# Performance work log

Hardware: AMD Instinct MI355X
Metric: run time of the kernel (lower is better)

## Reference

```python
import jax, jax.numpy as jnp
import numpy as np

N, H, F, E, K = 4096, 512, 2048, 8, 2  # tokens, hidden, ffn(=4H), experts, top_k


def setup_inputs() -> dict:
    key = jax.random.key(0)
    ks = jax.random.split(key, 7)
    def w(k, shape, fan_in):
        return jax.random.normal(k, shape, dtype=jnp.float32) * (fan_in ** -0.5)
    return {
        "x": jax.random.normal(ks[0], (N, H), dtype=jnp.float32),
        "W_in": w(ks[1], (H, H), H),          # input_proj.weight  [out,in]
        "W_router": w(ks[2], (E, H), H),      # router.gate.weight [E,H]
        "W_gate": w(ks[3], (E, F, H), H),     # per-expert gate_proj.weight
        "W_up": w(ks[4], (E, F, H), H),       # per-expert up_proj.weight
        "W_down": w(ks[5], (E, H, F), F),     # per-expert down_proj.weight
        "W_out": w(ks[6], (H, H), H),         # output_proj.weight
    }


def reference(x, W_in, W_router, W_gate, W_up, W_down, W_out):
    h = x @ W_in.T                                  # [N,H] input_proj
    logits = h @ W_router.T                         # [N,E]
    # route_mode='balanced' and world_size==1 -> expert_bias is None
    probs = jax.nn.softmax(logits, axis=-1)
    top_w, top_i = jax.lax.top_k(probs, K)          # [N,K]
    top_w = jax.nn.softmax(top_w, axis=-1)          # renormalize over top-k

    # per-token combine weight for each expert: [N,E]
    onehot = jax.nn.one_hot(top_i, E, dtype=h.dtype)      # [N,K,E]
    combine_w = jnp.einsum('nk,nke->ne', top_w, onehot)

    def expert(wg, wu, wd):
        # SwiGLU FFN: down( silu(gate(h)) * up(h) )
        return (jax.nn.silu(h @ wg.T) * (h @ wu.T)) @ wd.T  # [N,H]

    expert_out = jax.vmap(expert)(W_gate, W_up, W_down)     # [E,N,H]
    combined = jnp.einsum('ne,enh->nh', combine_w, expert_out)
    return combined @ W_out.T                                # output_proj
```

## Files before the change

kernel.cpp:

```cpp
#include <hip/hip_runtime.h>

typedef unsigned short u16;
typedef unsigned int u32;
typedef short bf16x8 __attribute__((ext_vector_type(8)));
typedef float f32x4 __attribute__((ext_vector_type(4)));

#define AS1 __attribute__((address_space(1)))
#define AS3 __attribute__((address_space(3)))

#define NTOK 4096
#define HDIM 512
#define FDIM 2048
#define NEXP 8
#define TOPK 2
#define NASSIGN (NTOK * TOPK)
#define NPAD (NASSIGN + NEXP * 128)
#define RBMAX 128

__device__ __forceinline__ void g2l16(const void* g, void* l) {
  __builtin_amdgcn_global_load_lds((const AS1 u32*)g, (AS3 u32*)l, 16, 0, 0);
}

__device__ __forceinline__ u16 f2bf(float f) {
  u32 u = __float_as_uint(f);
  u = (u + 0x7FFFu + ((u >> 16) & 1u)) >> 16;
  return (u16)u;
}

__global__ void cvt_kernel(const float* __restrict__ src, u16* __restrict__ dst, int n4) {
  int i = blockIdx.x * blockDim.x + threadIdx.x;
  if (i >= n4) return;
  float4 v = reinterpret_cast<const float4*>(src)[i];
  ushort4 o;
  o.x = f2bf(v.x); o.y = f2bf(v.y); o.z = f2bf(v.z); o.w = f2bf(v.w);
  reinterpret_cast<ushort4*>(dst)[i] = o;
}

__global__ void wreff_kernel(const float* __restrict__ Wr, const float* __restrict__ Win,
                             double* __restrict__ wre) {
  int t = blockIdx.x * blockDim.x + threadIdx.x;
  int e = t >> 9, k = t & 511;
  const float* wr = Wr + e * HDIM;
  double a = 0.0;
  for (int j = 0; j < HDIM; ++j) a += (double)wr[j] * (double)Win[j * HDIM + k];
  wre[t] = a;
}

__global__ __launch_bounds__(256) void router_kernel(
    const float* __restrict__ x, const double* __restrict__ wre,
    int* __restrict__ idx, float* __restrict__ wts) {
  __shared__ double lw[NEXP * HDIM];
  for (int i = threadIdx.x; i < NEXP * HDIM; i += 256) lw[i] = wre[i];
  __syncthreads();
  int n = blockIdx.x * 256 + threadIdx.x;
  const float* xr = x + (size_t)n * HDIM;
  double acc[NEXP] = {};
  for (int k = 0; k < HDIM; ++k) {
    double xv = (double)xr[k];
#pragma unroll
    for (int e = 0; e < NEXP; ++e) acc[e] += xv * lw[e * HDIM + k];
  }
  double mx = acc[0];
#pragma unroll
  for (int e = 1; e < NEXP; ++e) mx = acc[e] > mx ? acc[e] : mx;
  double p[NEXP], se = 0.0;
#pragma unroll
  for (int e = 0; e < NEXP; ++e) { p[e] = exp(acc[e] - mx); se += p[e]; }
  double inv = 1.0 / se;
#pragma unroll
  for (int e = 0; e < NEXP; ++e) p[e] *= inv;
  int i0 = 0; double b0 = p[0];
#pragma unroll
  for (int e = 1; e < NEXP; ++e) if (p[e] > b0) { b0 = p[e]; i0 = e; }
  int i1 = -1; double b1 = -1.0;
#pragma unroll
  for (int e = 0; e < NEXP; ++e) if (e != i0 && p[e] > b1) { b1 = p[e]; i1 = e; }
  double e0 = exp(b0), e1 = exp(b1);
  idx[2 * n] = i0; idx[2 * n + 1] = i1;
  wts[2 * n] = (float)(e0 / (e0 + e1));
  wts[2 * n + 1] = (float)(e1 / (e0 + e1));
}

__global__ void assign_kernel(const int* __restrict__ idx, int* __restrict__ tok,
                              int* __restrict__ pos, int* __restrict__ rbe,
                              int* __restrict__ rbp, int* __restrict__ nrb) {
  __shared__ int cnt[NEXP], cur[NEXP];
  const int tid = threadIdx.x;
  if (tid < NEXP) cnt[tid] = 0;
  __syncthreads();
  for (int a = tid; a < NASSIGN; a += 256) atomicAdd(&cnt[idx[a]], 1);
  __syncthreads();
  if (tid == 0) {
    int o = 0, n = 0;
    for (int e = 0; e < NEXP; ++e) {
      cur[e] = o;
      int nb = (cnt[e] + 127) >> 7;
      for (int i = 0; i < nb; ++i) { rbe[n] = e; rbp[n] = o + i * 128; ++n; }
      o += nb * 128;
    }
    nrb[0] = n;
  }
  __syncthreads();
  for (int p = tid; p < NPAD; p += 256) tok[p] = 0;
  __syncthreads();
  for (int a = tid; a < NASSIGN; a += 256) {
    int e = idx[a];
    int q = atomicAdd(&cur[e], 1);
    tok[q] = a >> 1;
    pos[a] = q;
  }
}

template <int STORE_BF16>
__global__ __launch_bounds__(256, 2) void gemm_bt_kernel(
    const u16* __restrict__ A, const u16* __restrict__ B, void* __restrict__ C,
    int M, int N, int K) {
  __shared__ u16 lA[128 * 64];
  __shared__ u16 lB[128 * 64];
  const int tid = threadIdx.x;
  const int w = tid >> 6, l = tid & 63;
  const int m0 = blockIdx.y * 128, n0 = blockIdx.x * 128;
  const int wm = (w >> 1) * 64, wn = (w & 1) * 64;
  const int lr = l >> 3, lc = (l & 7) * 8;
  f32x4 acc[4][4] = {};
  const u16* Ab = A + (size_t)(m0 + w * 32 + lr) * K + lc;
  const u16* Bb = B + (size_t)(n0 + w * 32 + lr) * K + lc;
  for (int kt = 0; kt < K; kt += 64) {
#pragma unroll
    for (int j = 0; j < 4; ++j) {
      g2l16(Ab + (size_t)j * 8 * K + kt, &lA[w * 2048 + j * 512]);
      g2l16(Bb + (size_t)j * 8 * K + kt, &lB[w * 2048 + j * 512]);
    }
    __syncthreads();
#pragma unroll
    for (int kk = 0; kk < 2; ++kk) {
      bf16x8 af[4], bf[4];
      const int ko = kk * 32 + (l >> 4) * 8;
#pragma unroll
      for (int i = 0; i < 4; ++i) af[i] = *(const bf16x8*)&lA[(wm + i * 16 + (l & 15)) * 64 + ko];
#pragma unroll
      for (int j = 0; j < 4; ++j) bf[j] = *(const bf16x8*)&lB[(wn + j * 16 + (l & 15)) * 64 + ko];
#pragma unroll
      for (int i = 0; i < 4; ++i)
#pragma unroll
        for (int j = 0; j < 4; ++j)
          acc[i][j] = __builtin_amdgcn_mfma_f32_16x16x32_bf16(af[i], bf[j], acc[i][j], 0, 0, 0);
    }
    __syncthreads();
  }
  const int cr = (l >> 4) * 4, cc = l & 15;
#pragma unroll
  for (int i = 0; i < 4; ++i)
#pragma unroll
    for (int j = 0; j < 4; ++j)
#pragma unroll
      for (int r = 0; r < 4; ++r) {
        int row = m0 + wm + i * 16 + cr + r;
        int col = n0 + wn + j * 16 + cc;
        if (STORE_BF16)
          ((u16*)C)[(size_t)row * N + col] = f2bf(acc[i][j][r]);
        else
          ((float*)C)[(size_t)row * N + col] = acc[i][j][r];
      }
}

__global__ __launch_bounds__(256, 2) void gateup_kernel(
    const u16* __restrict__ hb, const u16* __restrict__ Wg, const u16* __restrict__ Wu,
    u16* __restrict__ act, const int* __restrict__ tok, const int* __restrict__ rbe,
    const int* __restrict__ rbp, const int* __restrict__ nrb) {
  const int rb = blockIdx.y;
  if (rb >= nrb[0]) return;
  __shared__ u16 lA[128 * 64];
  __shared__ u16 lG[128 * 64];
  __shared__ u16 lU[128 * 64];
  const int e = rbe[rb], p0 = rbp[rb], n0 = blockIdx.x * 128;
  const int tid = threadIdx.x;
  const int w = tid >> 6, l = tid & 63;
  const int wm = (w >> 1) * 64, wn = (w & 1) * 64;
  const int lr = l >> 3, lc = (l & 7) * 8;
  const u16* Bg = Wg + (size_t)e * (FDIM * HDIM) + (size_t)(n0 + w * 32 + lr) * HDIM + lc;
  const u16* Bu = Wu + (size_t)e * (FDIM * HDIM) + (size_t)(n0 + w * 32 + lr) * HDIM + lc;
  int trow[4];
#pragma unroll
  for (int j = 0; j < 4; ++j) trow[j] = tok[p0 + w * 32 + j * 8 + lr];
  f32x4 ag[4][4] = {}, au[4][4] = {};
  for (int kt = 0; kt < HDIM; kt += 64) {
#pragma unroll
    for (int j = 0; j < 4; ++j) {
      g2l16(hb + (size_t)trow[j] * HDIM + kt + lc, &lA[w * 2048 + j * 512]);
      g2l16(Bg + (size_t)j * 8 * HDIM + kt, &lG[w * 2048 + j * 512]);
      g2l16(Bu + (size_t)j * 8 * HDIM + kt, &lU[w * 2048 + j * 512]);
    }
    __syncthreads();
#pragma unroll
    for (int kk = 0; kk < 2; ++kk) {
      bf16x8 af[4], gf[4], uf[4];
      const int ko = kk * 32 + (l >> 4) * 8;
#pragma unroll
      for (int i = 0; i < 4; ++i) af[i] = *(const bf16x8*)&lA[(wm + i * 16 + (l & 15)) * 64 + ko];
#pragma unroll
      for (int j = 0; j < 4; ++j) {
        gf[j] = *(const bf16x8*)&lG[(wn + j * 16 + (l & 15)) * 64 + ko];
        uf[j] = *(const bf16x8*)&lU[(wn + j * 16 + (l & 15)) * 64 + ko];
      }
#pragma unroll
      for (int i = 0; i < 4; ++i)
#pragma unroll
        for (int j = 0; j < 4; ++j) {
          ag[i][j] = __builtin_amdgcn_mfma_f32_16x16x32_bf16(af[i], gf[j], ag[i][j], 0, 0, 0);
          au[i][j] = __builtin_amdgcn_mfma_f32_16x16x32_bf16(af[i], uf[j], au[i][j], 0, 0, 0);
        }
    }
    __syncthreads();
  }
  const int cr = (l >> 4) * 4, cc = l & 15;
#pragma unroll
  for (int i = 0; i < 4; ++i)
#pragma unroll
    for (int j = 0; j < 4; ++j)
#pragma unroll
      for (int r = 0; r < 4; ++r) {
        int prow = p0 + wm + i * 16 + cr + r;
        int col = n0 + wn + j * 16 + cc;
        float g = ag[i][j][r], u = au[i][j][r];
        float s = g / (1.0f + __expf(-g));
        act[(size_t)prow * FDIM + col] = f2bf(s * u);
      }
}

__global__ __launch_bounds__(256, 2) void down_kernel(
    const u16* __restrict__ act, const u16* __restrict__ Wd, float* __restrict__ dout,
    const int* __restrict__ rbe, const int* __restrict__ rbp, const int* __restrict__ nrb) {
  const int rb = blockIdx.y;
  if (rb >= nrb[0]) return;
  __shared__ u16 lA[128 * 64];
  __shared__ u16 lB[128 * 64];
  const int e = rbe[rb], p0 = rbp[rb], n0 = blockIdx.x * 128;
  const int tid = threadIdx.x;
  const int w = tid >> 6, l = tid & 63;
  const int wm = (w >> 1) * 64, wn = (w & 1) * 64;
  const int lr = l >> 3, lc = (l & 7) * 8;
  f32x4 acc[4][4] = {};
  const u16* Ab = act + (size_t)(p0 + w * 32 + lr) * FDIM + lc;
  const u16* Bb = Wd + (size_t)e * (HDIM * FDIM) + (size_t)(n0 + w * 32 + lr) * FDIM + lc;
  for (int kt = 0; kt < FDIM; kt += 64) {
#pragma unroll
    for (int j = 0; j < 4; ++j) {
      g2l16(Ab + (size_t)j * 8 * FDIM + kt, &lA[w * 2048 + j * 512]);
      g2l16(Bb + (size_t)j * 8 * FDIM + kt, &lB[w * 2048 + j * 512]);
    }
    __syncthreads();
#pragma unroll
    for (int kk = 0; kk < 2; ++kk) {
      bf16x8 af[4], bf[4];
      const int ko = kk * 32 + (l >> 4) * 8;
#pragma unroll
      for (int i = 0; i < 4; ++i) af[i] = *(const bf16x8*)&lA[(wm + i * 16 + (l & 15)) * 64 + ko];
#pragma unroll
      for (int j = 0; j < 4; ++j) bf[j] = *(const bf16x8*)&lB[(wn + j * 16 + (l & 15)) * 64 + ko];
#pragma unroll
      for (int i = 0; i < 4; ++i)
#pragma unroll
        for (int j = 0; j < 4; ++j)
          acc[i][j] = __builtin_amdgcn_mfma_f32_16x16x32_bf16(af[i], bf[j], acc[i][j], 0, 0, 0);
    }
    __syncthreads();
  }
  const int cr = (l >> 4) * 4, cc = l & 15;
#pragma unroll
  for (int i = 0; i < 4; ++i)
#pragma unroll
    for (int j = 0; j < 4; ++j)
#pragma unroll
      for (int r = 0; r < 4; ++r) {
        int prow = p0 + wm + i * 16 + cr + r;
        int col = n0 + wn + j * 16 + cc;
        dout[(size_t)prow * HDIM + col] = acc[i][j][r];
      }
}

__global__ void combine_kernel(const float* __restrict__ dout, const int* __restrict__ pos,
                               const float* __restrict__ wts, u16* __restrict__ cb) {
  const int n = blockIdx.x, t = threadIdx.x;
  const int p0 = pos[2 * n], p1 = pos[2 * n + 1];
  const float w0 = wts[2 * n], w1 = wts[2 * n + 1];
  const float4 a = reinterpret_cast<const float4*>(dout + (size_t)p0 * HDIM)[t];
  const float4 b = reinterpret_cast<const float4*>(dout + (size_t)p1 * HDIM)[t];
  ushort4 o;
  o.x = f2bf(w0 * a.x + w1 * b.x);
  o.y = f2bf(w0 * a.y + w1 * b.y);
  o.z = f2bf(w0 * a.z + w1 * b.z);
  o.w = f2bf(w0 * a.w + w1 * b.w);
  reinterpret_cast<ushort4*>(cb + (size_t)n * HDIM)[t] = o;
}

extern "C" void kernel_launch(void* const* d_in, const int* in_sizes, int n_in,
                              void* d_out, int out_size, void* d_ws, size_t ws_size,
                              hipStream_t stream) {
  const float* x   = (const float*)d_in[0];
  const float* Wi  = (const float*)d_in[1];
  const float* Wr  = (const float*)d_in[2];
  const float* Wg  = (const float*)d_in[3];
  const float* Wu  = (const float*)d_in[4];
  const float* Wd  = (const float*)d_in[5];
  const float* Wo  = (const float*)d_in[6];
  float* out = (float*)d_out;

  char* ws = (char*)d_ws;
  size_t off = 0;
  auto alloc = [&](size_t bytes) -> void* {
    off = (off + 255) & ~(size_t)255;
    void* p = ws + off;
    off += bytes;
    return p;
  };
  u16* xb  = (u16*)alloc((size_t)NTOK * HDIM * 2);
  u16* hb  = (u16*)alloc((size_t)NTOK * HDIM * 2);
  u16* cb  = (u16*)alloc((size_t)NTOK * HDIM * 2);
  u16* Wib = (u16*)alloc((size_t)HDIM * HDIM * 2);
  u16* Wob = (u16*)alloc((size_t)HDIM * HDIM * 2);
  u16* Wgb = (u16*)alloc((size_t)NEXP * FDIM * HDIM * 2);
  u16* Wub = (u16*)alloc((size_t)NEXP * FDIM * HDIM * 2);
  u16* Wdb = (u16*)alloc((size_t)NEXP * HDIM * FDIM * 2);
  u16* actb = (u16*)alloc((size_t)NPAD * FDIM * 2);
  float* dwn = (float*)alloc((size_t)NPAD * HDIM * 4);
  double* wre = (double*)alloc((size_t)NEXP * HDIM * 8);
  int* idx = (int*)alloc((size_t)NASSIGN * 4);
  float* wts = (float*)alloc((size_t)NASSIGN * 4);
  int* tok = (int*)alloc((size_t)NPAD * 4);
  int* pos = (int*)alloc((size_t)NASSIGN * 4);
  int* rbe = (int*)alloc((size_t)RBMAX * 4);
  int* rbp = (int*)alloc((size_t)RBMAX * 4);
  int* nrb = (int*)alloc(256);

  auto cvt = [&](const float* s, u16* d, size_t n) {
    int n4 = (int)(n / 4);
    cvt_kernel<<<(n4 + 255) / 256, 256, 0, stream>>>(s, d, n4);
  };
  cvt(x, xb, (size_t)NTOK * HDIM);
  cvt(Wi, Wib, (size_t)HDIM * HDIM);
  cvt(Wg, Wgb, (size_t)NEXP * FDIM * HDIM);
  cvt(Wu, Wub, (size_t)NEXP * FDIM * HDIM);
  cvt(Wd, Wdb, (size_t)NEXP * HDIM * FDIM);
  cvt(Wo, Wob, (size_t)HDIM * HDIM);

  wreff_kernel<<<(NEXP * HDIM) / 256, 256, 0, stream>>>(Wr, Wi, wre);
  gemm_bt_kernel<1><<<dim3(HDIM / 128, NTOK / 128), 256, 0, stream>>>(xb, Wib, hb, NTOK, HDIM, HDIM);
  router_kernel<<<NTOK / 256, 256, 0, stream>>>(x, wre, idx, wts);
  assign_kernel<<<1, 256, 0, stream>>>(idx, tok, pos, rbe, rbp, nrb);
  gateup_kernel<<<dim3(FDIM / 128, 72), 256, 0, stream>>>(hb, Wgb, Wub, actb, tok, rbe, rbp, nrb);
  down_kernel<<<dim3(HDIM / 128, 72), 256, 0, stream>>>(actb, Wdb, dwn, rbe, rbp, nrb);
  combine_kernel<<<NTOK, 128, 0, stream>>>(dwn, pos, wts, cb);
  gemm_bt_kernel<0><<<dim3(HDIM / 128, NTOK / 128), 256, 0, stream>>>(cb, Wob, out, NTOK, HDIM, HDIM);
}
```

Baseline: 251.5 us.

## Fuse prep kernels, double-buffer GEMMs with swizzled LDS, store down output in bf16

Merges the separate conversion, router-weight, input-projection and router launches into two multi-role prep kernels, so independent work shares one launch. Rewrites all GEMMs to use 512-thread blocks, double-buffered LDS with an XOR swizzle, and a prefetch of the next k-tile during MFMA compute. The down projection now covers a wider 256-column tile and stores bf16 instead of fp32, which halves the intermediate traffic that combine reads. In exchange the down output carries extra rounding, and each block needs more LDS.

```diff
diff --git a/kernel.cpp b/kernel.cpp
--- a/kernel.cpp
+++ b/kernel.cpp
@@ -12,73 +12,166 @@
 #define HDIM 512
 #define FDIM 2048
 #define NEXP 8
-#define TOPK 2
-#define NASSIGN (NTOK * TOPK)
+#define NASSIGN (NTOK * 2)
 #define NPAD (NASSIGN + NEXP * 128)
 #define RBMAX 128
 
 __device__ __forceinline__ void g2l16(const void* g, void* l) {
   __builtin_amdgcn_global_load_lds((const AS1 u32*)g, (AS3 u32*)l, 16, 0, 0);
 }
-
 __device__ __forceinline__ u16 f2bf(float f) {
   u32 u = __float_as_uint(f);
   u = (u + 0x7FFFu + ((u >> 16) & 1u)) >> 16;
   return (u16)u;
 }
-
-__global__ void cvt_kernel(const float* __restrict__ src, u16* __restrict__ dst, int n4) {
-  int i = blockIdx.x * blockDim.x + threadIdx.x;
-  if (i >= n4) return;
-  float4 v = reinterpret_cast<const float4*>(src)[i];
-  ushort4 o;
-  o.x = f2bf(v.x); o.y = f2bf(v.y); o.z = f2bf(v.z); o.w = f2bf(v.w);
-  reinterpret_cast<ushort4*>(dst)[i] = o;
-}
-
-__global__ void wreff_kernel(const float* __restrict__ Wr, const float* __restrict__ Win,
-                             double* __restrict__ wre) {
-  int t = blockIdx.x * blockDim.x + threadIdx.x;
-  int e = t >> 9, k = t & 511;
-  const float* wr = Wr + e * HDIM;
-  double a = 0.0;
-  for (int j = 0; j < HDIM; ++j) a += (double)wr[j] * (double)Win[j * HDIM + k];
-  wre[t] = a;
-}
-
-__global__ __launch_bounds__(256) void router_kernel(
+__device__ __forceinline__ float bf2f(u16 h) { return __uint_as_float(((u32)h) << 16); }
+
+#define VMBAR() do { asm volatile("s_waitcnt vmcnt(0)" ::: "memory"); __builtin_amdgcn_s_barrier(); } while (0)
+
+__global__ __launch_bounds__(512, 4) void prep1_kernel(
+    const float* __restrict__ x, const float* __restrict__ Wi, const float* __restrict__ Wo,
+    const float* __restrict__ Wr, u16* __restrict__ xb, u16* __restrict__ Wib,
+    u16* __restrict__ Wob, double* __restrict__ wre) {
+  const int b = blockIdx.x, tid = threadIdx.x;
+  if (b < 640) {
+    const float* s; u16* d; int base;
+    if (b < 512) { s = x; d = xb; base = b * 1024; }
+    else if (b < 576) { s = Wi; d = Wib; base = (b - 512) * 1024; }
+    else { s = Wo; d = Wob; base = (b - 576) * 1024; }
+#pragma unroll
+    for (int i = 0; i < 2; ++i) {
+      const int ix = base + tid + i * 512;
+      const float4 v = ((const float4*)s)[ix];
+      ushort4 o; o.x = f2bf(v.x); o.y = f2bf(v.y); o.z = f2bf(v.z); o.w = f2bf(v.w);
+      ((ushort4*)d)[ix] = o;
+    }
+  } else {
+    const int t = (b - 640) * 512 + tid;
+    const int e = t >> 9, k = t & 511;
+    const float* wr = Wr + e * HDIM;
+    double a = 0.0;
+    for (int j = 0; j < HDIM; ++j) a += (double)wr[j] * (double)Wi[j * HDIM + k];
+    wre[t] = a;
+  }
+}
+
+template <int SB, int NT>
+__device__ __forceinline__ void gemm128_body(
+    const u16* __restrict__ A, const u16* __restrict__ B, void* __restrict__ C,
+    int m0, int n0, int N, int K, u16* sm, int tid) {
+  u16 *lA0 = sm, *lA1 = sm + 8192, *lB0 = sm + 16384, *lB1 = sm + 24576;
+  const int w = tid >> 6, l = tid & 63;
+  const int wm = (w >> 2) * 64, wn = (w & 3) * 32;
+  const int lm = l & 15, lk = (l >> 4) * 8, xr = (l & 7) << 3;
+  const int sr = l >> 3, sc = ((l & 7) ^ sr) * 8;
+  const u16* As = A + (size_t)(m0 + w * 8 + sr) * K + sc;
+  const u16* Bs = B + (size_t)(n0 + w * 8 + sr) * K + sc;
+  f32x4 acc[4][2] = {};
+  auto STG = [&](u16* dA, u16* dB, int kt) {
+    g2l16(As + kt, dA + w * 512);
+    g2l16(As + (size_t)64 * K + kt, dA + 4096 + w * 512);
+    g2l16(Bs + kt, dB + w * 512);
+    g2l16(Bs + (size_t)64 * K + kt, dB + 4096 + w * 512);
+  };
+  auto CMP = [&](const u16* a_, const u16* b_) {
+#pragma unroll
+    for (int kk = 0; kk < 2; ++kk) {
+      const int ko = (kk * 32 + lk) ^ xr;
+      bf16x8 af[4], bf[2];
+#pragma unroll
+      for (int i = 0; i < 4; ++i) af[i] = *(const bf16x8*)(a_ + (wm + i * 16 + lm) * 64 + ko);
+#pragma unroll
+      for (int j = 0; j < 2; ++j) bf[j] = *(const bf16x8*)(b_ + (wn + j * 16 + lm) * 64 + ko);
+#pragma unroll
+      for (int i = 0; i < 4; ++i)
+#pragma unroll
+        for (int j = 0; j < 2; ++j)
+          acc[i][j] = __builtin_amdgcn_mfma_f32_16x16x32_bf16(af[i], bf[j], acc[i][j], 0, 0, 0);
+    }
+  };
+  STG(lA0, lB0, 0);
+  VMBAR();
+  for (int t = 0; t < NT; t += 2) {
+    if (t + 1 < NT) STG(lA1, lB1, (t + 1) * 64);
+    CMP(lA0, lB0);
+    VMBAR();
+    if (t + 2 < NT) STG(lA0, lB0, (t + 2) * 64);
+    CMP(lA1, lB1);
+    VMBAR();
+  }
+  const int cr = (l >> 4) * 4, cc = lm;
+#pragma unroll
+  for (int i = 0; i < 4; ++i)
+#pragma unroll
+    for (int j = 0; j < 2; ++j)
+#pragma unroll
+      for (int r = 0; r < 4; ++r) {
+        const size_t o = (size_t)(m0 + wm + i * 16 + cr + r) * N + n0 + wn + j * 16 + cc;
+        if (SB) ((u16*)C)[o] = f2bf(acc[i][j][r]);
+        else ((float*)C)[o] = acc[i][j][r];
+      }
+}
+
+__global__ __launch_bounds__(512, 4) void prep2_kernel(
     const float* __restrict__ x, const double* __restrict__ wre,
+    const u16* __restrict__ xb, const u16* __restrict__ Wib,
+    const float* __restrict__ Wg, const float* __restrict__ Wu, const float* __restrict__ Wd,
+    u16* __restrict__ hb, u16* __restrict__ Wgb, u16* __restrict__ Wub, u16* __restrict__ Wdb,
     int* __restrict__ idx, float* __restrict__ wts) {
-  __shared__ double lw[NEXP * HDIM];
-  for (int i = threadIdx.x; i < NEXP * HDIM; i += 256) lw[i] = wre[i];
-  __syncthreads();
-  int n = blockIdx.x * 256 + threadIdx.x;
-  const float* xr = x + (size_t)n * HDIM;
-  double acc[NEXP] = {};
-  for (int k = 0; k < HDIM; ++k) {
-    double xv = (double)xr[k];
-#pragma unroll
-    for (int e = 0; e < NEXP; ++e) acc[e] += xv * lw[e * HDIM + k];
-  }
-  double mx = acc[0];
-#pragma unroll
-  for (int e = 1; e < NEXP; ++e) mx = acc[e] > mx ? acc[e] : mx;
-  double p[NEXP], se = 0.0;
-#pragma unroll
-  for (int e = 0; e < NEXP; ++e) { p[e] = exp(acc[e] - mx); se += p[e]; }
-  double inv = 1.0 / se;
-#pragma unroll
-  for (int e = 0; e < NEXP; ++e) p[e] *= inv;
-  int i0 = 0; double b0 = p[0];
-#pragma unroll
-  for (int e = 1; e < NEXP; ++e) if (p[e] > b0) { b0 = p[e]; i0 = e; }
-  int i1 = -1; double b1 = -1.0;
-#pragma unroll
-  for (int e = 0; e < NEXP; ++e) if (e != i0 && p[e] > b1) { b1 = p[e]; i1 = e; }
-  double e0 = exp(b0), e1 = exp(b1);
-  idx[2 * n] = i0; idx[2 * n + 1] = i1;
-  wts[2 * n] = (float)(e0 / (e0 + e1));
-  wts[2 * n + 1] = (float)(e1 / (e0 + e1));
+  __shared__ __align__(16) u16 pp[32768];
+  const int b = blockIdx.x, tid = threadIdx.x;
+  if (b < 8) {
+    double* lw = (double*)pp;
+    for (int i = tid; i < NEXP * HDIM; i += 512) lw[i] = wre[i];
+    __syncthreads();
+    const int n = b * 512 + tid;
+    const float* xr = x + (size_t)n * HDIM;
+    double acc[NEXP] = {};
+    for (int k4 = 0; k4 < HDIM / 4; ++k4) {
+      const float4 xv = ((const float4*)xr)[k4];
+      const float xc[4] = {xv.x, xv.y, xv.z, xv.w};
+#pragma unroll
+      for (int c = 0; c < 4; ++c) {
+        const double xd = (double)xc[c];
+#pragma unroll
+        for (int e = 0; e < NEXP; ++e) acc[e] += xd * lw[e * HDIM + k4 * 4 + c];
+      }
+    }
+    double mx = acc[0];
+#pragma unroll
+    for (int e = 1; e < NEXP; ++e) mx = acc[e] > mx ? acc[e] : mx;
+    double p[NEXP], se = 0.0;
+#pragma unroll
+    for (int e = 0; e < NEXP; ++e) { p[e] = exp(acc[e] - mx); se += p[e]; }
+    const double inv = 1.0 / se;
+#pragma unroll
+    for (int e = 0; e < NEXP; ++e) p[e] *= inv;
+    int i0 = 0; double b0 = p[0];
+#pragma unroll
+    for (int e = 1; e < NEXP; ++e) if (p[e] > b0) { b0 = p[e]; i0 = e; }
+    int i1 = -1; double b1 = -1.0;
+#pragma unroll
+    for (int e = 0; e < NEXP; ++e) if (e != i0 && p[e] > b1) { b1 = p[e]; i1 = e; }
+    const double e0 = exp(b0), e1 = exp(b1);
+    idx[2 * n] = i0; idx[2 * n + 1] = i1;
+    wts[2 * n] = (float)(e0 / (e0 + e1));
+    wts[2 * n + 1] = (float)(e1 / (e0 + e1));
+  } else if (b < 136) {
+    const int g = b - 8;
+    gemm128_body<1, 8>(xb, Wib, hb, (g >> 2) * 128, (g & 3) * 128, HDIM, HDIM, pp, tid);
+  } else {
+    const int cb = b - 136, which = cb >> 9, lb = cb & 511;
+    const float* s = which == 0 ? Wg : which == 1 ? Wu : Wd;
+    u16* d = which == 0 ? Wgb : which == 1 ? Wub : Wdb;
+    const int base = lb * 4096 + tid;
+#pragma unroll
+    for (int i = 0; i < 8; ++i) {
+      const int ix = base + i * 512;
+      const float4 v = ((const float4*)s)[ix];
+      ushort4 o; o.x = f2bf(v.x); o.y = f2bf(v.y); o.z = f2bf(v.z); o.w = f2bf(v.w);
+      ((ushort4*)d)[ix] = o;
+    }
+  }
 }
 
 __global__ void assign_kernel(const int* __restrict__ idx, int* __restrict__ tok,
@@ -94,7 +187,7 @@
     int o = 0, n = 0;
     for (int e = 0; e < NEXP; ++e) {
       cur[e] = o;
-      int nb = (cnt[e] + 127) >> 7;
+      const int nb = (cnt[e] + 127) >> 7;
       for (int i = 0; i < nb; ++i) { rbe[n] = e; rbp[n] = o + i * 128; ++n; }
       o += nb * 128;
     }
@@ -104,206 +197,176 @@
   for (int p = tid; p < NPAD; p += 256) tok[p] = 0;
   __syncthreads();
   for (int a = tid; a < NASSIGN; a += 256) {
-    int e = idx[a];
-    int q = atomicAdd(&cur[e], 1);
+    const int e = idx[a];
+    const int q = atomicAdd(&cur[e], 1);
     tok[q] = a >> 1;
     pos[a] = q;
   }
 }
 
-template <int STORE_BF16>
-__global__ __launch_bounds__(256, 2) void gemm_bt_kernel(
-    const u16* __restrict__ A, const u16* __restrict__ B, void* __restrict__ C,
-    int M, int N, int K) {
-  __shared__ u16 lA[128 * 64];
-  __shared__ u16 lB[128 * 64];
-  const int tid = threadIdx.x;
-  const int w = tid >> 6, l = tid & 63;
-  const int m0 = blockIdx.y * 128, n0 = blockIdx.x * 128;
-  const int wm = (w >> 1) * 64, wn = (w & 1) * 64;
-  const int lr = l >> 3, lc = (l & 7) * 8;
-  f32x4 acc[4][4] = {};
-  const u16* Ab = A + (size_t)(m0 + w * 32 + lr) * K + lc;
-  const u16* Bb = B + (size_t)(n0 + w * 32 + lr) * K + lc;
-  for (int kt = 0; kt < K; kt += 64) {
-#pragma unroll
-    for (int j = 0; j < 4; ++j) {
-      g2l16(Ab + (size_t)j * 8 * K + kt, &lA[w * 2048 + j * 512]);
-      g2l16(Bb + (size_t)j * 8 * K + kt, &lB[w * 2048 + j * 512]);
-    }
-    __syncthreads();
-#pragma unroll
-    for (int kk = 0; kk < 2; ++kk) {
-      bf16x8 af[4], bf[4];
-      const int ko = kk * 32 + (l >> 4) * 8;
-#pragma unroll
-      for (int i = 0; i < 4; ++i) af[i] = *(const bf16x8*)&lA[(wm + i * 16 + (l & 15)) * 64 + ko];
-#pragma unroll
-      for (int j = 0; j < 4; ++j) bf[j] = *(const bf16x8*)&lB[(wn + j * 16 + (l & 15)) * 64 + ko];
-#pragma unroll
-      for (int i = 0; i < 4; ++i)
-#pragma unroll
-        for (int j = 0; j < 4; ++j)
-          acc[i][j] = __builtin_amdgcn_mfma_f32_16x16x32_bf16(af[i], bf[j], acc[i][j], 0, 0, 0);
-    }
-    __syncthreads();
-  }
-  const int cr = (l >> 4) * 4, cc = l & 15;
-#pragma unroll
-  for (int i = 0; i < 4; ++i)
-#pragma unroll
-    for (int j = 0; j < 4; ++j)
-#pragma unroll
-      for (int r = 0; r < 4; ++r) {
-        int row = m0 + wm + i * 16 + cr + r;
-        int col = n0 + wn + j * 16 + cc;
-        if (STORE_BF16)
-          ((u16*)C)[(size_t)row * N + col] = f2bf(acc[i][j][r]);
-        else
-          ((float*)C)[(size_t)row * N + col] = acc[i][j][r];
-      }
-}
-
-__global__ __launch_bounds__(256, 2) void gateup_kernel(
+__global__ __launch_bounds__(512, 2) void gateup_kernel(
     const u16* __restrict__ hb, const u16* __restrict__ Wg, const u16* __restrict__ Wu,
     u16* __restrict__ act, const int* __restrict__ tok, const int* __restrict__ rbe,
     const int* __restrict__ rbp, const int* __restrict__ nrb) {
   const int rb = blockIdx.y;
   if (rb >= nrb[0]) return;
-  __shared__ u16 lA[128 * 64];
-  __shared__ u16 lG[128 * 64];
-  __shared__ u16 lU[128 * 64];
+  __shared__ __align__(16) u16 sm[49152];
+  u16 *lA0 = sm, *lA1 = sm + 8192, *lG0 = sm + 16384, *lG1 = sm + 24576,
+      *lU0 = sm + 32768, *lU1 = sm + 40960;
   const int e = rbe[rb], p0 = rbp[rb], n0 = blockIdx.x * 128;
-  const int tid = threadIdx.x;
-  const int w = tid >> 6, l = tid & 63;
-  const int wm = (w >> 1) * 64, wn = (w & 1) * 64;
-  const int lr = l >> 3, lc = (l & 7) * 8;
-  const u16* Bg = Wg + (size_t)e * (FDIM * HDIM) + (size_t)(n0 + w * 32 + lr) * HDIM + lc;
-  const u16* Bu = Wu + (size_t)e * (FDIM * HDIM) + (size_t)(n0 + w * 32 + lr) * HDIM + lc;
-  int trow[4];
-#pragma unroll
-  for (int j = 0; j < 4; ++j) trow[j] = tok[p0 + w * 32 + j * 8 + lr];
-  f32x4 ag[4][4] = {}, au[4][4] = {};
-  for (int kt = 0; kt < HDIM; kt += 64) {
-#pragma unroll
-    for (int j = 0; j < 4; ++j) {
-      g2l16(hb + (size_t)trow[j] * HDIM + kt + lc, &lA[w * 2048 + j * 512]);
-      g2l16(Bg + (size_t)j * 8 * HDIM + kt, &lG[w * 2048 + j * 512]);
-      g2l16(Bu + (size_t)j * 8 * HDIM + kt, &lU[w * 2048 + j * 512]);
-    }
-    __syncthreads();
+  const int tid = threadIdx.x, w = tid >> 6, l = tid & 63;
+  const int wm = (w >> 2) * 64, wn = (w & 3) * 32;
+  const int lm = l & 15, lk = (l >> 4) * 8, xr = (l & 7) << 3;
+  const int sr = l >> 3, sc = ((l & 7) ^ sr) * 8;
+  const u16* A0 = hb + (size_t)tok[p0 + w * 8 + sr] * HDIM + sc;
+  const u16* A1 = hb + (size_t)tok[p0 + 64 + w * 8 + sr] * HDIM + sc;
+  const u16* G0 = Wg + (size_t)e * FDIM * HDIM + (size_t)(n0 + w * 8 + sr) * HDIM + sc;
+  const u16* G1 = G0 + (size_t)64 * HDIM;
+  const u16* U0 = Wu + (size_t)e * FDIM * HDIM + (size_t)(n0 + w * 8 + sr) * HDIM + sc;
+  const u16* U1 = U0 + (size_t)64 * HDIM;
+  f32x4 ag[4][2] = {}, au[4][2] = {};
+  auto STG = [&](u16* dA, u16* dG, u16* dU, int kt) {
+    g2l16(A0 + kt, dA + w * 512);
+    g2l16(A1 + kt, dA + 4096 + w * 512);
+    g2l16(G0 + kt, dG + w * 512);
+    g2l16(G1 + kt, dG + 4096 + w * 512);
+    g2l16(U0 + kt, dU + w * 512);
+    g2l16(U1 + kt, dU + 4096 + w * 512);
+  };
+  auto CMP = [&](const u16* a_, const u16* g_, const u16* u_) {
 #pragma unroll
     for (int kk = 0; kk < 2; ++kk) {
-      bf16x8 af[4], gf[4], uf[4];
-      const int ko = kk * 32 + (l >> 4) * 8;
-#pragma unroll
-      for (int i = 0; i < 4; ++i) af[i] = *(const bf16x8*)&lA[(wm + i * 16 + (l & 15)) * 64 + ko];
-#pragma unroll
-      for (int j = 0; j < 4; ++j) {
-        gf[j] = *(const bf16x8*)&lG[(wn + j * 16 + (l & 15)) * 64 + ko];
-        uf[j] = *(const bf16x8*)&lU[(wn + j * 16 + (l & 15)) * 64 + ko];
+      const int ko = (kk * 32 + lk) ^ xr;
+      bf16x8 af[4], gf[2], uf[2];
+#pragma unroll
+      for (int i = 0; i < 4; ++i) af[i] = *(const bf16x8*)(a_ + (wm + i * 16 + lm) * 64 + ko);
+#pragma unroll
+      for (int j = 0; j < 2; ++j) {
+        gf[j] = *(const bf16x8*)(g_ + (wn + j * 16 + lm) * 64 + ko);
+        uf[j] = *(const bf16x8*)(u_ + (wn + j * 16 + lm) * 64 + ko);
       }
 #pragma unroll
       for (int i = 0; i < 4; ++i)
 #pragma unroll
-        for (int j = 0; j < 4; ++j) {
+        for (int j = 0; j < 2; ++j) {
           ag[i][j] = __builtin_amdgcn_mfma_f32_16x16x32_bf16(af[i], gf[j], ag[i][j], 0, 0, 0);
           au[i][j] = __builtin_amdgcn_mfma_f32_16x16x32_bf16(af[i], uf[j], au[i][j], 0, 0, 0);
         }
     }
-    __syncthreads();
-  }
-  const int cr = (l >> 4) * 4, cc = l & 15;
+  };
+  STG(lA0, lG0, lU0, 0);
+  VMBAR();
+#pragma unroll
+  for (int t = 0; t < 8; t += 2) {
+    if (t + 1 < 8) STG(lA1, lG1, lU1, (t + 1) * 64);
+    CMP(lA0, lG0, lU0);
+    VMBAR();
+    if (t + 2 < 8) STG(lA0, lG0, lU0, (t + 2) * 64);
+    CMP(lA1, lG1, lU1);
+    VMBAR();
+  }
+  const int cr = (l >> 4) * 4, cc = lm;
 #pragma unroll
   for (int i = 0; i < 4; ++i)
 #pragma unroll
-    for (int j = 0; j < 4; ++j)
+    for (int j = 0; j < 2; ++j)
 #pragma unroll
       for (int r = 0; r < 4; ++r) {
-        int prow = p0 + wm + i * 16 + cr + r;
-        int col = n0 + wn + j * 16 + cc;
-        float g = ag[i][j][r], u = au[i][j][r];
-        float s = g / (1.0f + __expf(-g));
-        act[(size_t)prow * FDIM + col] = f2bf(s * u);
+        const float g = ag[i][j][r], u = au[i][j][r];
+        const float s = g / (1.0f + __expf(-g));
+        act[(size_t)(p0 + wm + i * 16 + cr + r) * FDIM + n0 + wn + j * 16 + cc] = f2bf(s * u);
       }
 }
 
-__global__ __launch_bounds__(256, 2) void down_kernel(
-    const u16* __restrict__ act, const u16* __restrict__ Wd, float* __restrict__ dout,
+__global__ __launch_bounds__(512, 2) void down_kernel(
+    const u16* __restrict__ act, const u16* __restrict__ Wd, u16* __restrict__ dwn,
     const int* __restrict__ rbe, const int* __restrict__ rbp, const int* __restrict__ nrb) {
   const int rb = blockIdx.y;
   if (rb >= nrb[0]) return;
-  __shared__ u16 lA[128 * 64];
-  __shared__ u16 lB[128 * 64];
-  const int e = rbe[rb], p0 = rbp[rb], n0 = blockIdx.x * 128;
-  const int tid = threadIdx.x;
-  const int w = tid >> 6, l = tid & 63;
-  const int wm = (w >> 1) * 64, wn = (w & 1) * 64;
-  const int lr = l >> 3, lc = (l & 7) * 8;
+  __shared__ __align__(16) u16 sm[49152];
+  u16 *lA0 = sm, *lA1 = sm + 8192, *lB0 = sm + 16384, *lB1 = sm + 32768;
+  const int e = rbe[rb], p0 = rbp[rb], n0 = blockIdx.x * 256;
+  const int tid = threadIdx.x, w = tid >> 6, l = tid & 63;
+  const int wm = (w >> 2) * 64, wn = (w & 3) * 64;
+  const int lm = l & 15, lk = (l >> 4) * 8, xr = (l & 7) << 3;
+  const int sr = l >> 3, sc = ((l & 7) ^ sr) * 8;
+  const u16* As = act + (size_t)(p0 + w * 8 + sr) * FDIM + sc;
+  const u16* Bs = Wd + (size_t)e * HDIM * FDIM + (size_t)(n0 + w * 8 + sr) * FDIM + sc;
   f32x4 acc[4][4] = {};
-  const u16* Ab = act + (size_t)(p0 + w * 32 + lr) * FDIM + lc;
-  const u16* Bb = Wd + (size_t)e * (HDIM * FDIM) + (size_t)(n0 + w * 32 + lr) * FDIM + lc;
-  for (int kt = 0; kt < FDIM; kt += 64) {
-#pragma unroll
-    for (int j = 0; j < 4; ++j) {
-      g2l16(Ab + (size_t)j * 8 * FDIM + kt, &lA[w * 2048 + j * 512]);
-      g2l16(Bb + (size_t)j * 8 * FDIM + kt, &lB[w * 2048 + j * 512]);
-    }
-    __syncthreads();
+  auto STG = [&](u16* dA, u16* dB, int kt) {
+    g2l16(As + kt, dA + w * 512);
+    g2l16(As + (size_t)64 * FDIM + kt, dA + 4096 + w * 512);
+#pragma unroll
+    for (int c = 0; c < 4; ++c)
+      g2l16(Bs + (size_t)(64 * c) * FDIM + kt, dB + c * 4096 + w * 512);
+  };
+  auto CMP = [&](const u16* a_, const u16* b_) {
 #pragma unroll
     for (int kk = 0; kk < 2; ++kk) {
+      const int ko = (kk * 32 + lk) ^ xr;
       bf16x8 af[4], bf[4];
-      const int ko = kk * 32 + (l >> 4) * 8;
-#pragma unroll
-      for (int i = 0; i < 4; ++i) af[i] = *(const bf16x8*)&lA[(wm + i * 16 + (l & 15)) * 64 + ko];
-#pragma unroll
-      for (int j = 0; j < 4; ++j) bf[j] = *(const bf16x8*)&lB[(wn + j * 16 + (l & 15)) * 64 + ko];
+#pragma unroll
+      for (int i = 0; i < 4; ++i) af[i] = *(const bf16x8*)(a_ + (wm + i * 16 + lm) * 64 + ko);
+#pragma unroll
+      for (int j = 0; j < 4; ++j) bf[j] = *(const bf16x8*)(b_ + (wn + j * 16 + lm) * 64 + ko);
 #pragma unroll
       for (int i = 0; i < 4; ++i)
 #pragma unroll
         for (int j = 0; j < 4; ++j)
           acc[i][j] = __builtin_amdgcn_mfma_f32_16x16x32_bf16(af[i], bf[j], acc[i][j], 0, 0, 0);
     }
-    __syncthreads();
-  }
-  const int cr = (l >> 4) * 4, cc = l & 15;
+  };
+  STG(lA0, lB0, 0);
+  VMBAR();
+  for (int t = 0; t < 32; t += 2) {
+    if (t + 1 < 32) STG(lA1, lB1, (t + 1) * 64);
+    CMP(lA0, lB0);
+    VMBAR();
+    if (t + 2 < 32) STG(lA0, lB0, (t + 2) * 64);
+    CMP(lA1, lB1);
+    VMBAR();
+  }
+  const int cr = (l >> 4) * 4, cc = lm;
 #pragma unroll
   for (int i = 0; i < 4; ++i)
 #pragma unroll
     for (int j = 0; j < 4; ++j)
 #pragma unroll
-      for (int r = 0; r < 4; ++r) {
-        int prow = p0 + wm + i * 16 + cr + r;
-        int col = n0 + wn + j * 16 + cc;
-        dout[(size_t)prow * HDIM + col] = acc[i][j][r];
-      }
-}
-
-__global__ void combine_kernel(const float* __restrict__ dout, const int* __restrict__ pos,
+      for (int r = 0; r < 4; ++r)
+        dwn[(size_t)(p0 + wm + i * 16 + cr + r) * HDIM + n0 + wn + j * 16 + cc] = f2bf(acc[i][j][r]);
+}
+
+__global__ void combine_kernel(const u16* __restrict__ dwn, const int* __restrict__ pos,
                                const float* __restrict__ wts, u16* __restrict__ cb) {
   const int n = blockIdx.x, t = threadIdx.x;
   const int p0 = pos[2 * n], p1 = pos[2 * n + 1];
   const float w0 = wts[2 * n], w1 = wts[2 * n + 1];
-  const float4 a = reinterpret_cast<const float4*>(dout + (size_t)p0 * HDIM)[t];
-  const float4 b = reinterpret_cast<const float4*>(dout + (size_t)p1 * HDIM)[t];
+  const ushort4 a = ((const ushort4*)(dwn + (size_t)p0 * HDIM))[t];
+  const ushort4 b = ((const ushort4*)(dwn + (size_t)p1 * HDIM))[t];
   ushort4 o;
-  o.x = f2bf(w0 * a.x + w1 * b.x);
-  o.y = f2bf(w0 * a.y + w1 * b.y);
-  o.z = f2bf(w0 * a.z + w1 * b.z);
-  o.w = f2bf(w0 * a.w + w1 * b.w);
-  reinterpret_cast<ushort4*>(cb + (size_t)n * HDIM)[t] = o;
+  o.x = f2bf(w0 * bf2f(a.x) + w1 * bf2f(b.x));
+  o.y = f2bf(w0 * bf2f(a.y) + w1 * bf2f(b.y));
+  o.z = f2bf(w0 * bf2f(a.z) + w1 * bf2f(b.z));
+  o.w = f2bf(w0 * bf2f(a.w) + w1 * bf2f(b.w));
+  ((ushort4*)(cb + (size_t)n * HDIM))[t] = o;
+}
+
+__global__ __launch_bounds__(512, 4) void out_gemm_kernel(
+    const u16* __restrict__ cb, const u16* __restrict__ Wob, float* __restrict__ out) {
+  __shared__ __align__(16) u16 sm[32768];
+  gemm128_body<0, 8>(cb, Wob, out, blockIdx.y * 128, blockIdx.x * 128, HDIM, HDIM, sm, threadIdx.x);
 }
 
 extern "C" void kernel_launch(void* const* d_in, const int* in_sizes, int n_in,
                               void* d_out, int out_size, void* d_ws, size_t ws_size,
                               hipStream_t stream) {
-  const float* x   = (const float*)d_in[0];
-  const float* Wi  = (const float*)d_in[1];
-  const float* Wr  = (const float*)d_in[2];
-  const float* Wg  = (const float*)d_in[3];
-  const float* Wu  = (const float*)d_in[4];
-  const float* Wd  = (const float*)d_in[5];
-  const float* Wo  = (const float*)d_in[6];
+  const float* x  = (const float*)d_in[0];
+  const float* Wi = (const float*)d_in[1];
+  const float* Wr = (const float*)d_in[2];
+  const float* Wg = (const float*)d_in[3];
+  const float* Wu = (const float*)d_in[4];
+  const float* Wd = (const float*)d_in[5];
+  const float* Wo = (const float*)d_in[6];
   float* out = (float*)d_out;
 
   char* ws = (char*)d_ws;
@@ -323,7 +386,7 @@
   u16* Wub = (u16*)alloc((size_t)NEXP * FDIM * HDIM * 2);
   u16* Wdb = (u16*)alloc((size_t)NEXP * HDIM * FDIM * 2);
   u16* actb = (u16*)alloc((size_t)NPAD * FDIM * 2);
-  float* dwn = (float*)alloc((size_t)NPAD * HDIM * 4);
+  u16* dwn = (u16*)alloc((size_t)NPAD * HDIM * 2);
   double* wre = (double*)alloc((size_t)NEXP * HDIM * 8);
   int* idx = (int*)alloc((size_t)NASSIGN * 4);
   float* wts = (float*)alloc((size_t)NASSIGN * 4);
@@ -333,23 +396,11 @@
   int* rbp = (int*)alloc((size_t)RBMAX * 4);
   int* nrb = (int*)alloc(256);
 
-  auto cvt = [&](const float* s, u16* d, size_t n) {
-    int n4 = (int)(n / 4);
-    cvt_kernel<<<(n4 + 255) / 256, 256, 0, stream>>>(s, d, n4);
-  };
-  cvt(x, xb, (size_t)NTOK * HDIM);
-  cvt(Wi, Wib, (size_t)HDIM * HDIM);
-  cvt(Wg, Wgb, (size_t)NEXP * FDIM * HDIM);
-  cvt(Wu, Wub, (size_t)NEXP * FDIM * HDIM);
-  cvt(Wd, Wdb, (size_t)NEXP * HDIM * FDIM);
-  cvt(Wo, Wob, (size_t)HDIM * HDIM);
-
-  wreff_kernel<<<(NEXP * HDIM) / 256, 256, 0, stream>>>(Wr, Wi, wre);
-  gemm_bt_kernel<1><<<dim3(HDIM / 128, NTOK / 128), 256, 0, stream>>>(xb, Wib, hb, NTOK, HDIM, HDIM);
-  router_kernel<<<NTOK / 256, 256, 0, stream>>>(x, wre, idx, wts);
+  prep1_kernel<<<648, 512, 0, stream>>>(x, Wi, Wo, Wr, xb, Wib, Wob, wre);
+  prep2_kernel<<<1672, 512, 0, stream>>>(x, wre, xb, Wib, Wg, Wu, Wd, hb, Wgb, Wub, Wdb, idx, wts);
   assign_kernel<<<1, 256, 0, stream>>>(idx, tok, pos, rbe, rbp, nrb);
-  gateup_kernel<<<dim3(FDIM / 128, 72), 256, 0, stream>>>(hb, Wgb, Wub, actb, tok, rbe, rbp, nrb);
-  down_kernel<<<dim3(HDIM / 128, 72), 256, 0, stream>>>(actb, Wdb, dwn, rbe, rbp, nrb);
+  gateup_kernel<<<dim3(16, 72), 512, 0, stream>>>(hb, Wgb, Wub, actb, tok, rbe, rbp, nrb);
+  down_kernel<<<dim3(2, 72), 512, 0, stream>>>(actb, Wdb, dwn, rbe, rbp, nrb);
   combine_kernel<<<NTOK, 128, 0, stream>>>(dwn, pos, wts, cb);
-  gemm_bt_kernel<0><<<dim3(HDIM / 128, NTOK / 128), 256, 0, stream>>>(cb, Wob, out, NTOK, HDIM, HDIM);
-}
+  out_gemm_kernel<<<dim3(4, 32), 512, 0, stream>>>(cb, Wob, out);
+}
```

New measurement: 218.5 us. -13.1%, faster.
